# Kernel tuning notes

Hardware: AMD Instinct MI355X
Metric: run time of the kernel (lower is better)

## Reference

```python
import jax, jax.numpy as jnp
import numpy as np

N, C_IN, H, W = 1024, 22, 19, 19
C_TRUNK, HID, NHIST = 384, 128, 5
HIST_START = 9  # channels 9..13 hold move history planes


def setup_inputs() -> dict:
    key = jax.random.key(0)
    ks = jax.random.split(key, 8)
    return {
        "input_spatial": jax.random.uniform(ks[0], (N, C_IN, H, W), dtype=jnp.float32),
        "trunk_out": jax.random.normal(ks[1], (N, C_TRUNK, H, W), dtype=jnp.float32),
        "w_ih": jax.random.normal(ks[2], (4 * HID, C_TRUNK), dtype=jnp.float32) * 0.05,
        "w_hh": jax.random.normal(ks[3], (4 * HID, HID), dtype=jnp.float32) * 0.05,
        "b_ih": jax.random.normal(ks[4], (4 * HID,), dtype=jnp.float32) * 0.05,
        "b_hh": jax.random.normal(ks[5], (4 * HID,), dtype=jnp.float32) * 0.05,
        "w_proj": jax.random.normal(ks[6], (C_TRUNK, HID), dtype=jnp.float32) * 0.05,
        "b_proj": jax.random.normal(ks[7], (C_TRUNK,), dtype=jnp.float32) * 0.05,
    }


def reference(input_spatial, trunk_out, w_ih, w_hh, b_ih, b_hh, w_proj, b_proj):
    n, _, h, w = input_spatial.shape
    c_trunk = trunk_out.shape[1]
    # --- extract_move_coords (vectorized) ---
    planes = input_spatial[:, HIST_START:HIST_START + NHIST]          # N,5,H,W
    flat = planes.reshape(n, NHIST, h * w)                            # N,5,HW
    has_move = flat.sum(axis=-1) > 0.5                                # N,5 bool
    idx = jnp.argmax(flat, axis=-1)                                   # N,5 (== r*W+c; clamp(-1,min=0)==0 handled by mask)
    # --- gather trunk features at move coords, mask missing moves ---
    trunk_flat = trunk_out.reshape(n, c_trunk, h * w)                 # N,Ct,HW
    feats = jnp.take_along_axis(trunk_flat, idx[:, None, :], axis=2)  # N,Ct,5
    feats = feats.transpose(0, 2, 1) * has_move[..., None].astype(trunk_out.dtype)  # N,5,Ct
    seq = feats[:, ::-1, :]                                           # oldest -> newest
    # --- single-layer LSTM (torch gate order: i, f, g, o) ---
    def step(carry, x_t):
        h_t, c_t = carry
        g = x_t @ w_ih.T + h_t @ w_hh.T + b_ih + b_hh                 # N,4H
        i_g, f_g, g_g, o_g = jnp.split(g, 4, axis=-1)
        c_new = jax.nn.sigmoid(f_g) * c_t + jax.nn.sigmoid(i_g) * jnp.tanh(g_g)
        h_new = jax.nn.sigmoid(o_g) * jnp.tanh(c_new)
        return (h_new, c_new), None

    h0 = jnp.zeros((n, HID), dtype=seq.dtype)
    (h_final, _), _ = jax.lax.scan(step, (h0, h0), seq.transpose(1, 0, 2))
    out = h_final @ w_proj.T + b_proj                                 # N,Ct
    return out[:, :, None, None]                                      # N,Ct,1,1
```

## Files before the change

### kernel.cpp

```cpp
#include <hip/hip_runtime.h>
#include <hip/hip_bf16.h>
#include <float.h>

#define N_SAMP   1024
#define C_IN     22
#define HW       361
#define C_TRUNK  384
#define HID      128
#define NHIST    5
#define HIST_START 9
#define NGATE    512

typedef __attribute__((ext_vector_type(8))) short short8v;
typedef __attribute__((ext_vector_type(4))) float float4v;

static __device__ __forceinline__ ushort f2bf(float x) {
  unsigned int b = __float_as_uint(x);
  b += 0x7fffu + ((b >> 16) & 1u);
  return (ushort)(b >> 16);
}

__global__ __launch_bounds__(320) void argmax_kernel(
    const float* __restrict__ inp,
    int*   __restrict__ idxb,
    float* __restrict__ movb)
{
  const int n    = blockIdx.x;
  const int wave = threadIdx.x >> 6;
  const int lane = threadIdx.x & 63;

  const float* base = inp + ((size_t)n * C_IN + HIST_START + wave) * HW;
  float v = -FLT_MAX; int vi = 0; float sum = 0.f;
  #pragma unroll
  for (int r = 0; r < 6; ++r) {
    int i = lane + r * 64;
    if (i < HW) {
      float x = base[i];
      sum += x;
      if (x > v) { v = x; vi = i; }
    }
  }
  #pragma unroll
  for (int m = 1; m < 64; m <<= 1) {
    float v2 = __shfl_xor(v, m);
    int   i2 = __shfl_xor(vi, m);
    float s2 = __shfl_xor(sum, m);
    if (v2 > v || (v2 == v && i2 < vi)) { v = v2; vi = i2; }
    sum += s2;
  }
  if (lane == 0) {
    idxb[n * NHIST + wave] = vi;
    movb[n * NHIST + wave] = (sum > 0.5f) ? 1.f : 0.f;
  }
}

__global__ __launch_bounds__(384) void gather_kernel(
    const float* __restrict__ trunk,
    const int*   __restrict__ idxb,
    const float* __restrict__ movb,
    ushort* __restrict__ seq)
{
  const int n = blockIdx.x;
  const int c = threadIdx.x;

  const int   i0 = idxb[n * NHIST + 4], i1 = idxb[n * NHIST + 3],
              i2 = idxb[n * NHIST + 2], i3 = idxb[n * NHIST + 1],
              i4 = idxb[n * NHIST + 0];
  const float m0 = movb[n * NHIST + 4], m1 = movb[n * NHIST + 3],
              m2 = movb[n * NHIST + 2], m3 = movb[n * NHIST + 1],
              m4 = movb[n * NHIST + 0];

  const float* tb = trunk + ((size_t)n * C_TRUNK + c) * HW;
  float x0 = tb[i0], x1 = tb[i1], x2 = tb[i2], x3 = tb[i3], x4 = tb[i4];

  ushort* so = seq + (size_t)n * NHIST * C_TRUNK + c;
  so[0 * C_TRUNK] = f2bf(x0 * m0);
  so[1 * C_TRUNK] = f2bf(x1 * m1);
  so[2 * C_TRUNK] = f2bf(x2 * m2);
  so[3 * C_TRUNK] = f2bf(x3 * m3);
  so[4 * C_TRUNK] = f2bf(x4 * m4);
}

__global__ __launch_bounds__(256) void gates_kernel(
    const ushort* __restrict__ seq,
    const float* __restrict__ w_ih,
    const float* __restrict__ b_ih,
    const float* __restrict__ b_hh,
    float* __restrict__ G)
{
  __shared__ ushort As[64][40];
  __shared__ ushort Bs[64][40];
  const int tid  = threadIdx.x;
  const int wv   = tid >> 6;
  const int lane = tid & 63;
  const int m0 = blockIdx.y * 64;
  const int j0 = blockIdx.x * 64;
  const int row_l = tid >> 2;
  const int koff  = (tid & 3) * 8;

  float4v acc0 = {0.f,0.f,0.f,0.f};
  float4v acc1 = {0.f,0.f,0.f,0.f};
  float4v acc2 = {0.f,0.f,0.f,0.f};
  float4v acc3 = {0.f,0.f,0.f,0.f};

  const int fr = lane & 15;
  const int fk = (lane >> 4) * 8;

  for (int k0 = 0; k0 < C_TRUNK; k0 += 32) {
    *(short8v*)&As[row_l][koff] =
        *(const short8v*)(seq + (size_t)(m0 + row_l) * C_TRUNK + k0 + koff);
    const float* wp = w_ih + (size_t)(j0 + row_l) * C_TRUNK + k0 + koff;
    float4 w0 = *(const float4*)wp;
    float4 w1 = *(const float4*)(wp + 4);
    short8v bvec;
    bvec[0] = (short)f2bf(w0.x); bvec[1] = (short)f2bf(w0.y);
    bvec[2] = (short)f2bf(w0.z); bvec[3] = (short)f2bf(w0.w);
    bvec[4] = (short)f2bf(w1.x); bvec[5] = (short)f2bf(w1.y);
    bvec[6] = (short)f2bf(w1.z); bvec[7] = (short)f2bf(w1.w);
    *(short8v*)&Bs[row_l][koff] = bvec;
    __syncthreads();

    short8v af  = *(const short8v*)&As[wv * 16 + fr][fk];
    short8v bf0 = *(const short8v*)&Bs[ 0 + fr][fk];
    short8v bf1 = *(const short8v*)&Bs[16 + fr][fk];
    short8v bf2 = *(const short8v*)&Bs[32 + fr][fk];
    short8v bf3 = *(const short8v*)&Bs[48 + fr][fk];
    acc0 = __builtin_amdgcn_mfma_f32_16x16x32_bf16(af, bf0, acc0, 0, 0, 0);
    acc1 = __builtin_amdgcn_mfma_f32_16x16x32_bf16(af, bf1, acc1, 0, 0, 0);
    acc2 = __builtin_amdgcn_mfma_f32_16x16x32_bf16(af, bf2, acc2, 0, 0, 0);
    acc3 = __builtin_amdgcn_mfma_f32_16x16x32_bf16(af, bf3, acc3, 0, 0, 0);
    __syncthreads();
  }

  const int rbase = m0 + wv * 16 + (lane >> 4) * 4;
  #pragma unroll
  for (int j = 0; j < 4; ++j) {
    const float4v a = (j == 0) ? acc0 : (j == 1) ? acc1 : (j == 2) ? acc2 : acc3;
    const int cj = j0 + j * 16 + fr;
    const float bsum = b_ih[cj] + b_hh[cj];
    #pragma unroll
    for (int r = 0; r < 4; ++r)
      G[(size_t)(rbase + r) * NGATE + cj] = a[r] + bsum;
  }
}

__global__ __launch_bounds__(512, 2) void lstm_kernel(
    const float* __restrict__ G,
    const float* __restrict__ w_hh,
    const float* __restrict__ w_proj,
    const float* __restrict__ b_proj,
    float* __restrict__ out)
{
  const int n0  = blockIdx.x * 4;
  const int tid = threadIdx.x;
  const int g   = tid >> 7;
  const int j   = tid & 127;

  __shared__ float hs[4][HID];
  __shared__ float glds[4][4][HID];

  float gpre[NHIST][4];
  #pragma unroll
  for (int t = 0; t < NHIST; ++t)
    #pragma unroll
    for (int s = 0; s < 4; ++s)
      gpre[t][s] = G[((size_t)(n0 + s) * NHIST + t) * NGATE + tid];

  float4 wreg[32];
  #pragma unroll
  for (int k4 = 0; k4 < 32; ++k4)
    wreg[k4] = *(const float4*)(w_hh + (size_t)(g * HID + j) * HID + k4 * 4);

  hs[g][j] = 0.f;
  float c = 0.f;
  __syncthreads();

  #pragma unroll
  for (int t = 0; t < NHIST; ++t) {
    float a[4];
    #pragma unroll
    for (int s = 0; s < 4; ++s) a[s] = gpre[t][s];

    #pragma unroll
    for (int k4 = 0; k4 < 32; ++k4) {
      float4 w = wreg[k4];
      #pragma unroll
      for (int s = 0; s < 4; ++s) {
        float4 h = *(const float4*)&hs[s][k4 * 4];
        a[s] += w.x * h.x + w.y * h.y + w.z * h.z + w.w * h.w;
      }
    }
    #pragma unroll
    for (int s = 0; s < 4; ++s) glds[g][s][j] = a[s];
    __syncthreads();
    {
      float ig = glds[0][g][j];
      float fg = glds[1][g][j];
      float gg = glds[2][g][j];
      float og = glds[3][g][j];
      ig = 1.f / (1.f + __expf(-ig));
      fg = 1.f / (1.f + __expf(-fg));
      og = 1.f / (1.f + __expf(-og));
      c  = fg * c + ig * tanhf(gg);
      hs[g][j] = og * tanhf(c);
    }
    __syncthreads();
  }

  if (tid < C_TRUNK) {
    const int cc = tid;
    const float4* wp = (const float4*)(w_proj + (size_t)cc * HID);
    float b = b_proj[cc];
    float po[4] = {b, b, b, b};
    #pragma unroll 8
    for (int k4 = 0; k4 < 32; ++k4) {
      float4 w  = wp[k4];
      float4 h0 = *(const float4*)&hs[0][k4 * 4];
      float4 h1 = *(const float4*)&hs[1][k4 * 4];
      float4 h2 = *(const float4*)&hs[2][k4 * 4];
      float4 h3 = *(const float4*)&hs[3][k4 * 4];
      po[0] += w.x*h0.x + w.y*h0.y + w.z*h0.z + w.w*h0.w;
      po[1] += w.x*h1.x + w.y*h1.y + w.z*h1.z + w.w*h1.w;
      po[2] += w.x*h2.x + w.y*h2.y + w.z*h2.z + w.w*h2.w;
      po[3] += w.x*h3.x + w.y*h3.y + w.z*h3.z + w.w*h3.w;
    }
    #pragma unroll
    for (int s = 0; s < 4; ++s)
      out[(size_t)(n0 + s) * C_TRUNK + cc] = po[s];
  }
}

extern "C" void kernel_launch(void* const* d_in, const int* in_sizes, int n_in,
                              void* d_out, int out_size, void* d_ws, size_t ws_size,
                              hipStream_t stream) {
  const float* inp    = (const float*)d_in[0];
  const float* trunk  = (const float*)d_in[1];
  const float* w_ih   = (const float*)d_in[2];
  const float* w_hh   = (const float*)d_in[3];
  const float* b_ih   = (const float*)d_in[4];
  const float* b_hh   = (const float*)d_in[5];
  const float* w_proj = (const float*)d_in[6];
  const float* b_proj = (const float*)d_in[7];
  float* out = (float*)d_out;

  char* ws = (char*)d_ws;
  int*    idxb = (int*)ws;
  float*  movb = (float*)(ws + 20480);
  ushort* seq  = (ushort*)(ws + 40960);
  float*  G    = (float*)(ws + 40960 +
                  (size_t)N_SAMP * NHIST * C_TRUNK * sizeof(ushort));

  argmax_kernel<<<N_SAMP, 320, 0, stream>>>(inp, idxb, movb);
  gather_kernel<<<N_SAMP, 384, 0, stream>>>(trunk, idxb, movb, seq);
  gates_kernel<<<dim3(NGATE / 64, (N_SAMP * NHIST) / 64), 256, 0, stream>>>(
      seq, w_ih, b_ih, b_hh, G);
  lstm_kernel<<<N_SAMP / 4, 512, 0, stream>>>(G, w_hh, w_proj, b_proj, out);
}
```

Measured before the change: 86.33 us.

## Fuse trunk gather into gates GEMM and pre-convert w_ih to bf16 in argmax kernel

Removes the separate gather kernel and its bf16 seq buffer: the gates GEMM now reads trunk values directly at the argmax indices, applies the move mask, converts to bf16, and prefetches the next k-slice into registers. The w_ih fp32 to bf16 conversion moves into the argmax kernel, so the GEMM loads pre-converted weights. This saves one launch and the seq write/read round trip. The trade-off is that each of the 8 column blocks re-gathers the same scattered trunk elements, multiplying uncoalesced strided loads.

```diff
diff --git a/kernel.cpp b/kernel.cpp
--- a/kernel.cpp
+++ b/kernel.cpp
@@ -22,12 +22,20 @@
 
 __global__ __launch_bounds__(320) void argmax_kernel(
     const float* __restrict__ inp,
-    int*   __restrict__ idxb,
-    float* __restrict__ movb)
+    const float* __restrict__ w_ih,
+    int*    __restrict__ idxb,
+    float*  __restrict__ movb,
+    ushort* __restrict__ w_ihb)
 {
   const int n    = blockIdx.x;
-  const int wave = threadIdx.x >> 6;
-  const int lane = threadIdx.x & 63;
+  const int tid  = threadIdx.x;
+  const int wave = tid >> 6;
+  const int lane = tid & 63;
+
+  if (n < 768 && tid < 256) {
+    int o = n * 256 + tid;
+    w_ihb[o] = f2bf(w_ih[o]);
+  }
 
   const float* base = inp + ((size_t)n * C_IN + HIST_START + wave) * HW;
   float v = -FLT_MAX; int vi = 0; float sum = 0.f;
@@ -54,38 +62,13 @@
   }
 }
 
-__global__ __launch_bounds__(384) void gather_kernel(
-    const float* __restrict__ trunk,
-    const int*   __restrict__ idxb,
-    const float* __restrict__ movb,
-    ushort* __restrict__ seq)
-{
-  const int n = blockIdx.x;
-  const int c = threadIdx.x;
-
-  const int   i0 = idxb[n * NHIST + 4], i1 = idxb[n * NHIST + 3],
-              i2 = idxb[n * NHIST + 2], i3 = idxb[n * NHIST + 1],
-              i4 = idxb[n * NHIST + 0];
-  const float m0 = movb[n * NHIST + 4], m1 = movb[n * NHIST + 3],
-              m2 = movb[n * NHIST + 2], m3 = movb[n * NHIST + 1],
-              m4 = movb[n * NHIST + 0];
-
-  const float* tb = trunk + ((size_t)n * C_TRUNK + c) * HW;
-  float x0 = tb[i0], x1 = tb[i1], x2 = tb[i2], x3 = tb[i3], x4 = tb[i4];
-
-  ushort* so = seq + (size_t)n * NHIST * C_TRUNK + c;
-  so[0 * C_TRUNK] = f2bf(x0 * m0);
-  so[1 * C_TRUNK] = f2bf(x1 * m1);
-  so[2 * C_TRUNK] = f2bf(x2 * m2);
-  so[3 * C_TRUNK] = f2bf(x3 * m3);
-  so[4 * C_TRUNK] = f2bf(x4 * m4);
-}
-
 __global__ __launch_bounds__(256) void gates_kernel(
-    const ushort* __restrict__ seq,
-    const float* __restrict__ w_ih,
-    const float* __restrict__ b_ih,
-    const float* __restrict__ b_hh,
+    const float*  __restrict__ trunk,
+    const ushort* __restrict__ w_ihb,
+    const int*    __restrict__ idxb,
+    const float*  __restrict__ movb,
+    const float*  __restrict__ b_ih,
+    const float*  __restrict__ b_hh,
     float* __restrict__ G)
 {
   __shared__ ushort As[64][40];
@@ -98,6 +81,12 @@
   const int row_l = tid >> 2;
   const int koff  = (tid & 3) * 8;
 
+  const int r  = m0 + row_l;
+  const int nn = r / 5;
+  const int tt = r - nn * 5;
+  const int   ip = idxb[nn * NHIST + 4 - tt];
+  const float mr = movb[nn * NHIST + 4 - tt];
+
   float4v acc0 = {0.f,0.f,0.f,0.f};
   float4v acc1 = {0.f,0.f,0.f,0.f};
   float4v acc2 = {0.f,0.f,0.f,0.f};
@@ -106,19 +95,27 @@
   const int fr = lane & 15;
   const int fk = (lane >> 4) * 8;
 
+  float va[8];
+  {
+    const float* tp = trunk + ((size_t)nn * C_TRUNK + koff) * HW + ip;
+    #pragma unroll
+    for (int q = 0; q < 8; ++q) va[q] = tp[q * HW];
+  }
+
   for (int k0 = 0; k0 < C_TRUNK; k0 += 32) {
-    *(short8v*)&As[row_l][koff] =
-        *(const short8v*)(seq + (size_t)(m0 + row_l) * C_TRUNK + k0 + koff);
-    const float* wp = w_ih + (size_t)(j0 + row_l) * C_TRUNK + k0 + koff;
-    float4 w0 = *(const float4*)wp;
-    float4 w1 = *(const float4*)(wp + 4);
-    short8v bvec;
-    bvec[0] = (short)f2bf(w0.x); bvec[1] = (short)f2bf(w0.y);
-    bvec[2] = (short)f2bf(w0.z); bvec[3] = (short)f2bf(w0.w);
-    bvec[4] = (short)f2bf(w1.x); bvec[5] = (short)f2bf(w1.y);
-    bvec[6] = (short)f2bf(w1.z); bvec[7] = (short)f2bf(w1.w);
-    *(short8v*)&Bs[row_l][koff] = bvec;
-    __syncthreads();
+    short8v avec;
+    #pragma unroll
+    for (int q = 0; q < 8; ++q) avec[q] = (short)f2bf(va[q] * mr);
+    *(short8v*)&As[row_l][koff] = avec;
+    *(short8v*)&Bs[row_l][koff] =
+        *(const short8v*)(w_ihb + (size_t)(j0 + row_l) * C_TRUNK + k0 + koff);
+    __syncthreads();
+
+    if (k0 + 32 < C_TRUNK) {
+      const float* tp = trunk + ((size_t)nn * C_TRUNK + k0 + 32 + koff) * HW + ip;
+      #pragma unroll
+      for (int q = 0; q < 8; ++q) va[q] = tp[q * HW];
+    }
 
     short8v af  = *(const short8v*)&As[wv * 16 + fr][fk];
     short8v bf0 = *(const short8v*)&Bs[ 0 + fr][fk];
@@ -139,8 +136,8 @@
     const int cj = j0 + j * 16 + fr;
     const float bsum = b_ih[cj] + b_hh[cj];
     #pragma unroll
-    for (int r = 0; r < 4; ++r)
-      G[(size_t)(rbase + r) * NGATE + cj] = a[r] + bsum;
+    for (int rr = 0; rr < 4; ++rr)
+      G[(size_t)(rbase + rr) * NGATE + cj] = a[rr] + bsum;
   }
 }
 
@@ -244,15 +241,13 @@
   float* out = (float*)d_out;
 
   char* ws = (char*)d_ws;
-  int*    idxb = (int*)ws;
-  float*  movb = (float*)(ws + 20480);
-  ushort* seq  = (ushort*)(ws + 40960);
-  float*  G    = (float*)(ws + 40960 +
-                  (size_t)N_SAMP * NHIST * C_TRUNK * sizeof(ushort));
-
-  argmax_kernel<<<N_SAMP, 320, 0, stream>>>(inp, idxb, movb);
-  gather_kernel<<<N_SAMP, 384, 0, stream>>>(trunk, idxb, movb, seq);
+  int*    idxb  = (int*)ws;
+  float*  movb  = (float*)(ws + 20480);
+  ushort* w_ihb = (ushort*)(ws + 40960);
+  float*  G     = (float*)(ws + 40960 + 393216);
+
+  argmax_kernel<<<N_SAMP, 320, 0, stream>>>(inp, w_ih, idxb, movb, w_ihb);
   gates_kernel<<<dim3(NGATE / 64, (N_SAMP * NHIST) / 64), 256, 0, stream>>>(
-      seq, w_ih, b_ih, b_hh, G);
+      trunk, w_ihb, idxb, movb, b_ih, b_hh, G);
   lstm_kernel<<<N_SAMP / 4, 512, 0, stream>>>(G, w_hh, w_proj, b_proj, out);
 }
```

New measurement: 268.0 us. +210.4%, slower.
